# Kernel optimization log

Hardware: AMD Instinct MI355X
Metric: run time of the kernel (lower is better)

The kernel has to match this reference:

```python
import jax, jax.numpy as jnp
import numpy as np

S, B, C = 7, 2, 20
LAMBDA_COORD = 5.0
LAMBDA_NOOBJ = 0.5
EPS = 1e-6


def setup_inputs() -> dict:
    key = jax.random.key(0)
    k1, k2 = jax.random.split(key)
    N = 16384
    predictions = jax.random.normal(k1, (N, S, S, B * 5 + C), dtype=jnp.float32)
    targets = jax.random.normal(k2, (N, S, S, B * 5 + C), dtype=jnp.float32)
    return {"predictions": predictions, "targets": targets}


def _iou(b1, b2):
    # b1: [..., B, 4], b2: [..., 1, 4]; boxes are (x, y, w, h)
    b1x1 = b1[..., 0] - b1[..., 2] / 2
    b1y1 = b1[..., 1] - b1[..., 3] / 2
    b1x2 = b1[..., 0] + b1[..., 2] / 2
    b1y2 = b1[..., 1] + b1[..., 3] / 2
    b2x1 = b2[..., 0] - b2[..., 2] / 2
    b2y1 = b2[..., 1] - b2[..., 3] / 2
    b2x2 = b2[..., 0] + b2[..., 2] / 2
    b2y2 = b2[..., 1] + b2[..., 3] / 2
    inter = jnp.clip(jnp.minimum(b1x2, b2x2) - jnp.maximum(b1x1, b2x1), 0, None) * \
            jnp.clip(jnp.minimum(b1y2, b2y2) - jnp.maximum(b1y1, b2y1), 0, None)
    union = b1[..., 2] * b1[..., 3] + b2[..., 2] * b2[..., 3] - inter
    return inter / (union + EPS)


def reference(predictions, targets):
    N = predictions.shape[0]
    pred_boxes = predictions[..., : B * 5].reshape(N, S, S, B, 5)  # [N,S,S,B,5]
    tgt_box = targets[..., :5]                                     # [N,S,S,5]

    ious = _iou(pred_boxes[..., :4], tgt_box[..., None, :4])       # [N,S,S,B]
    # Replicate loop semantics: best starts at (iou=0, idx=0), strict '>' update
    best_idx = jnp.argmax(jnp.where(ious > 0, ious, 0.0), axis=-1)  # [N,S,S]
    best_box = jnp.take_along_axis(
        pred_boxes, best_idx[..., None, None], axis=3
    )[..., 0, :]                                                    # [N,S,S,5]

    obj = (tgt_box[..., 4] > 0).astype(predictions.dtype)          # [N,S,S]

    # Localization loss
    xy_err = jnp.sum((best_box[..., :2] - tgt_box[..., :2]) ** 2, axis=-1)
    wh_err = jnp.sum(
        (jnp.sqrt(jnp.clip(best_box[..., 2:4], EPS, None)) -
         jnp.sqrt(jnp.clip(tgt_box[..., 2:4], EPS, None))) ** 2, axis=-1)
    coord_loss = jnp.sum(obj * (xy_err + wh_err)) / N

    # Confidence losses
    conf_obj_loss = jnp.sum(obj * (best_box[..., 4] - tgt_box[..., 4]) ** 2) / N
    conf_sq = pred_boxes[..., 4] ** 2                              # [N,S,S,B]
    conf_sq_all = jnp.sum(conf_sq, axis=-1)
    conf_sq_best = jnp.take_along_axis(conf_sq, best_idx[..., None], axis=-1)[..., 0]
    conf_noobj_loss = jnp.sum(obj * (conf_sq_all - conf_sq_best) +
                              (1.0 - obj) * conf_sq_all) / N

    # Classification loss (only for object cells)
    cls_err = jnp.sum((predictions[..., B * 5:] - targets[..., B * 5:]) ** 2, axis=-1)
    class_loss = jnp.sum(obj * cls_err) / N

    total = (LAMBDA_COORD * coord_loss + conf_obj_loss +
             LAMBDA_NOOBJ * conf_noobj_loss + class_loss)
    return total
```

## Files before the change

### kernel.cpp

```cpp
#include <hip/hip_runtime.h>


constexpr float LC   = 5.0f;
constexpr float LN   = 0.5f;
constexpr float EPSF = 1e-6f;

__device__ __forceinline__ float iou_pair(
    float cx1, float cy1, float w1, float h1,
    float cx2, float cy2, float w2, float h2) {
  float b1x1 = cx1 - w1 * 0.5f, b1x2 = cx1 + w1 * 0.5f;
  float b1y1 = cy1 - h1 * 0.5f, b1y2 = cy1 + h1 * 0.5f;
  float b2x1 = cx2 - w2 * 0.5f, b2x2 = cx2 + w2 * 0.5f;
  float b2y1 = cy2 - h2 * 0.5f, b2y2 = cy2 + h2 * 0.5f;
  float iw = fmaxf(fminf(b1x2, b2x2) - fmaxf(b1x1, b2x1), 0.0f);
  float ih = fmaxf(fminf(b1y2, b2y2) - fmaxf(b1y1, b2y1), 0.0f);
  float inter = iw * ih;
  float uni = w1 * h1 + w2 * h2 - inter;
  return inter / (uni + EPSF);
}

__global__ __launch_bounds__(256) void yolo_win_kernel(
    const float* __restrict__ pred, const float* __restrict__ tgt,
    float* __restrict__ partial, float invN) {
  const int tid  = threadIdx.x;
  const int cell = blockIdx.x * 256 + tid;
  const int odd  = cell & 1;

  const size_t wbase = (size_t)cell * 30 - 2 * odd;
  const float4* p4 = (const float4*)(pred + wbase);
  const float4* t4 = (const float4*)(tgt + wbase);

  float4 P0 = p4[0], P1 = p4[1], P2 = p4[2], P3 = p4[3];
  float4 P4_ = p4[4], P5 = p4[5], P6 = p4[6], P7 = p4[7];
  float4 T0 = t4[0], T1 = t4[1], T2 = t4[2], T3 = t4[3];
  float4 T4_ = t4[4], T5 = t4[5], T6 = t4[6], T7 = t4[7];

  float wp[32] = {P0.x,P0.y,P0.z,P0.w, P1.x,P1.y,P1.z,P1.w,
                  P2.x,P2.y,P2.z,P2.w, P3.x,P3.y,P3.z,P3.w,
                  P4_.x,P4_.y,P4_.z,P4_.w, P5.x,P5.y,P5.z,P5.w,
                  P6.x,P6.y,P6.z,P6.w, P7.x,P7.y,P7.z,P7.w};
  float wt[32] = {T0.x,T0.y,T0.z,T0.w, T1.x,T1.y,T1.z,T1.w,
                  T2.x,T2.y,T2.z,T2.w, T3.x,T3.y,T3.z,T3.w,
                  T4_.x,T4_.y,T4_.z,T4_.w, T5.x,T5.y,T5.z,T5.w,
                  T6.x,T6.y,T6.z,T6.w, T7.x,T7.y,T7.z,T7.w};

  float d2[32];
#pragma unroll
  for (int k = 0; k < 32; ++k) {
    float d = wp[k] - wt[k];
    d2[k] = d * d;
  }

  float s0 = (d2[0]+d2[1]) + (d2[2]+d2[3]);
  float s1 = (d2[4]+d2[5]) + (d2[6]+d2[7]);
  float s2 = (d2[8]+d2[9]) + (d2[10]+d2[11]);
  float s3 = (d2[12]+d2[13]) + (d2[14]+d2[15]);
  float s4 = (d2[16]+d2[17]) + (d2[18]+d2[19]);
  float s5 = (d2[20]+d2[21]) + (d2[22]+d2[23]);
  float s6 = (d2[24]+d2[25]) + (d2[26]+d2[27]);
  float s7 = (d2[28]+d2[29]) + (d2[30]+d2[31]);
  float total32 = ((s0+s1)+(s2+s3)) + ((s4+s5)+(s6+s7));

  float common = ((d2[0]+d2[1]) + (d2[2]+d2[3])) +
                 ((d2[4]+d2[5]) + (d2[6]+d2[7])) + (d2[8]+d2[9]);
  float extra  = odd ? (d2[10] + d2[11]) : (d2[30] + d2[31]);
  float cls = total32 - common - extra;

  float p0 = odd ? wp[2]  : wp[0];
  float p1 = odd ? wp[3]  : wp[1];
  float p2 = odd ? wp[4]  : wp[2];
  float p3 = odd ? wp[5]  : wp[3];
  float p4v= odd ? wp[6]  : wp[4];
  float p5 = odd ? wp[7]  : wp[5];
  float p6 = odd ? wp[8]  : wp[6];
  float p7 = odd ? wp[9]  : wp[7];
  float p8 = odd ? wp[10] : wp[8];
  float p9 = odd ? wp[11] : wp[9];
  float t0 = odd ? wt[2]  : wt[0];
  float t1 = odd ? wt[3]  : wt[1];
  float t2 = odd ? wt[4]  : wt[2];
  float t3 = odd ? wt[5]  : wt[3];
  float t4v= odd ? wt[6]  : wt[4];

  float iou0 = iou_pair(p0, p1, p2, p3, t0, t1, t2, t3);
  float iou1 = iou_pair(p5, p6, p7, p8, t0, t1, t2, t3);
  float v0 = iou0 > 0.0f ? iou0 : 0.0f;
  float v1 = iou1 > 0.0f ? iou1 : 0.0f;
  bool pick1 = v1 > v0;

  float bx = pick1 ? p5 : p0;
  float by = pick1 ? p6 : p1;
  float bw = pick1 ? p7 : p2;
  float bh = pick1 ? p8 : p3;
  float bc = pick1 ? p9 : p4v;

  float obj = t4v > 0.0f ? 1.0f : 0.0f;

  float dx = bx - t0, dy = by - t1;
  float xy = dx * dx + dy * dy;
  float sw = sqrtf(fmaxf(bw, EPSF)) - sqrtf(fmaxf(t2, EPSF));
  float sh = sqrtf(fmaxf(bh, EPSF)) - sqrtf(fmaxf(t3, EPSF));
  float wh = sw * sw + sh * sh;
  float dc = bc - t4v;

  float sq0 = p4v * p4v, sq1 = p9 * p9;
  float sq_all  = sq0 + sq1;
  float sq_best = pick1 ? sq1 : sq0;
  float noobj = obj * (sq_all - sq_best) + (1.0f - obj) * sq_all;

  float contrib = (obj * (LC * (xy + wh) + dc * dc + cls) + LN * noobj) * invN;

  for (int off = 32; off > 0; off >>= 1)
    contrib += __shfl_down(contrib, off);
  __shared__ float wsum[4];
  int lane = tid & 63;
  int wid  = tid >> 6;
  if (lane == 0) wsum[wid] = contrib;
  __syncthreads();
  if (tid == 0)
    partial[blockIdx.x] = (wsum[0] + wsum[1]) + (wsum[2] + wsum[3]);
}

__global__ __launch_bounds__(256) void yolo_final_kernel(
    const float* __restrict__ partial, int n, float* __restrict__ out) {
  double s = 0.0;
  for (int i = threadIdx.x; i < n; i += 256) s += (double)partial[i];
  for (int off = 32; off > 0; off >>= 1) s += __shfl_down(s, off);
  __shared__ double wsum[4];
  int lane = threadIdx.x & 63;
  int wid  = threadIdx.x >> 6;
  if (lane == 0) wsum[wid] = s;
  __syncthreads();
  if (threadIdx.x == 0)
    out[0] = (float)((wsum[0] + wsum[1]) + (wsum[2] + wsum[3]));
}

extern "C" void kernel_launch(void* const* d_in, const int* in_sizes, int n_in,
                              void* d_out, int out_size, void* d_ws, size_t ws_size,
                              hipStream_t stream) {
  const float* pred = (const float*)d_in[0];
  const float* tgt  = (const float*)d_in[1];
  float* out = (float*)d_out;
  float* partial = (float*)d_ws;

  int ncells  = in_sizes[0] / 30;
  int nblocks = ncells / 256;
  int N       = ncells / 49;
  float invN  = 1.0f / (float)N;

  yolo_win_kernel<<<nblocks, 256, 0, stream>>>(pred, tgt, partial, invN);
  yolo_final_kernel<<<1, 256, 0, stream>>>(partial, nblocks, out);
}
```

Before: 39.91 us.

## Split each cell's 32-float window across two lanes with shuffle-combined class sum

Each cell is now handled by two adjacent threads. Each thread loads half of the 128-byte window (four float4 from each input), and the two partial class-error sums are combined with a lane shuffle. Only the even lane computes the IoU and box loss terms. This doubles the thread count and halves per-thread loads and registers, aiming for more memory-level parallelism, at the cost of idle lanes during the box math and twice as many blocks and partials.

```diff
diff --git a/kernel.cpp b/kernel.cpp
--- a/kernel.cpp
+++ b/kernel.cpp
@@ -19,96 +19,94 @@
   return inter / (uni + EPSF);
 }
 
-__global__ __launch_bounds__(256) void yolo_win_kernel(
+__global__ __launch_bounds__(256) void yolo_duo_kernel(
     const float* __restrict__ pred, const float* __restrict__ tgt,
     float* __restrict__ partial, float invN) {
   const int tid  = threadIdx.x;
-  const int cell = blockIdx.x * 256 + tid;
+  const int gid  = blockIdx.x * 256 + tid;
+  const int s    = gid & 1;
+  const int cell = gid >> 1;
   const int odd  = cell & 1;
 
   const size_t wbase = (size_t)cell * 30 - 2 * odd;
-  const float4* p4 = (const float4*)(pred + wbase);
-  const float4* t4 = (const float4*)(tgt + wbase);
+  const float4* p4 = (const float4*)(pred + wbase) + 4 * s;
+  const float4* t4 = (const float4*)(tgt + wbase) + 4 * s;
 
   float4 P0 = p4[0], P1 = p4[1], P2 = p4[2], P3 = p4[3];
-  float4 P4_ = p4[4], P5 = p4[5], P6 = p4[6], P7 = p4[7];
   float4 T0 = t4[0], T1 = t4[1], T2 = t4[2], T3 = t4[3];
-  float4 T4_ = t4[4], T5 = t4[5], T6 = t4[6], T7 = t4[7];
 
-  float wp[32] = {P0.x,P0.y,P0.z,P0.w, P1.x,P1.y,P1.z,P1.w,
-                  P2.x,P2.y,P2.z,P2.w, P3.x,P3.y,P3.z,P3.w,
-                  P4_.x,P4_.y,P4_.z,P4_.w, P5.x,P5.y,P5.z,P5.w,
-                  P6.x,P6.y,P6.z,P6.w, P7.x,P7.y,P7.z,P7.w};
-  float wt[32] = {T0.x,T0.y,T0.z,T0.w, T1.x,T1.y,T1.z,T1.w,
-                  T2.x,T2.y,T2.z,T2.w, T3.x,T3.y,T3.z,T3.w,
-                  T4_.x,T4_.y,T4_.z,T4_.w, T5.x,T5.y,T5.z,T5.w,
-                  T6.x,T6.y,T6.z,T6.w, T7.x,T7.y,T7.z,T7.w};
+  float wp[16] = {P0.x,P0.y,P0.z,P0.w, P1.x,P1.y,P1.z,P1.w,
+                  P2.x,P2.y,P2.z,P2.w, P3.x,P3.y,P3.z,P3.w};
+  float wt[16] = {T0.x,T0.y,T0.z,T0.w, T1.x,T1.y,T1.z,T1.w,
+                  T2.x,T2.y,T2.z,T2.w, T3.x,T3.y,T3.z,T3.w};
 
-  float d2[32];
+  float d2[16];
 #pragma unroll
-  for (int k = 0; k < 32; ++k) {
+  for (int k = 0; k < 16; ++k) {
     float d = wp[k] - wt[k];
     d2[k] = d * d;
   }
 
-  float s0 = (d2[0]+d2[1]) + (d2[2]+d2[3]);
-  float s1 = (d2[4]+d2[5]) + (d2[6]+d2[7]);
-  float s2 = (d2[8]+d2[9]) + (d2[10]+d2[11]);
-  float s3 = (d2[12]+d2[13]) + (d2[14]+d2[15]);
-  float s4 = (d2[16]+d2[17]) + (d2[18]+d2[19]);
-  float s5 = (d2[20]+d2[21]) + (d2[22]+d2[23]);
-  float s6 = (d2[24]+d2[25]) + (d2[26]+d2[27]);
-  float s7 = (d2[28]+d2[29]) + (d2[30]+d2[31]);
-  float total32 = ((s0+s1)+(s2+s3)) + ((s4+s5)+(s6+s7));
+  float cls_part;
+  {
+    float hi6 = ((d2[10] + d2[11]) + (d2[12] + d2[13])) + (d2[14] + d2[15]);
+    float cls0 = odd ? (hi6 - d2[10] - d2[11]) : hi6;
+    float s0 = (d2[0] + d2[1]) + (d2[2] + d2[3]);
+    float s1 = (d2[4] + d2[5]) + (d2[6] + d2[7]);
+    float s2 = (d2[8] + d2[9]) + (d2[10] + d2[11]);
+    float s3 = (d2[12] + d2[13]) + (d2[14] + d2[15]);
+    float all16 = (s0 + s1) + (s2 + s3);
+    float cls1 = odd ? all16 : (all16 - d2[14] - d2[15]);
+    cls_part = s ? cls1 : cls0;
+  }
+  float cls = cls_part + __shfl_down(cls_part, 1);
 
-  float common = ((d2[0]+d2[1]) + (d2[2]+d2[3])) +
-                 ((d2[4]+d2[5]) + (d2[6]+d2[7])) + (d2[8]+d2[9]);
-  float extra  = odd ? (d2[10] + d2[11]) : (d2[30] + d2[31]);
-  float cls = total32 - common - extra;
+  float contrib = 0.0f;
+  if (s == 0) {
+    float p0 = odd ? wp[2]  : wp[0];
+    float p1 = odd ? wp[3]  : wp[1];
+    float p2 = odd ? wp[4]  : wp[2];
+    float p3 = odd ? wp[5]  : wp[3];
+    float p4v= odd ? wp[6]  : wp[4];
+    float p5 = odd ? wp[7]  : wp[5];
+    float p6 = odd ? wp[8]  : wp[6];
+    float p7 = odd ? wp[9]  : wp[7];
+    float p8 = odd ? wp[10] : wp[8];
+    float p9 = odd ? wp[11] : wp[9];
+    float t0 = odd ? wt[2]  : wt[0];
+    float t1 = odd ? wt[3]  : wt[1];
+    float t2 = odd ? wt[4]  : wt[2];
+    float t3 = odd ? wt[5]  : wt[3];
+    float t4v= odd ? wt[6]  : wt[4];
 
-  float p0 = odd ? wp[2]  : wp[0];
-  float p1 = odd ? wp[3]  : wp[1];
-  float p2 = odd ? wp[4]  : wp[2];
-  float p3 = odd ? wp[5]  : wp[3];
-  float p4v= odd ? wp[6]  : wp[4];
-  float p5 = odd ? wp[7]  : wp[5];
-  float p6 = odd ? wp[8]  : wp[6];
-  float p7 = odd ? wp[9]  : wp[7];
-  float p8 = odd ? wp[10] : wp[8];
-  float p9 = odd ? wp[11] : wp[9];
-  float t0 = odd ? wt[2]  : wt[0];
-  float t1 = odd ? wt[3]  : wt[1];
-  float t2 = odd ? wt[4]  : wt[2];
-  float t3 = odd ? wt[5]  : wt[3];
-  float t4v= odd ? wt[6]  : wt[4];
+    float iou0 = iou_pair(p0, p1, p2, p3, t0, t1, t2, t3);
+    float iou1 = iou_pair(p5, p6, p7, p8, t0, t1, t2, t3);
+    float v0 = iou0 > 0.0f ? iou0 : 0.0f;
+    float v1 = iou1 > 0.0f ? iou1 : 0.0f;
+    bool pick1 = v1 > v0;
 
-  float iou0 = iou_pair(p0, p1, p2, p3, t0, t1, t2, t3);
-  float iou1 = iou_pair(p5, p6, p7, p8, t0, t1, t2, t3);
-  float v0 = iou0 > 0.0f ? iou0 : 0.0f;
-  float v1 = iou1 > 0.0f ? iou1 : 0.0f;
-  bool pick1 = v1 > v0;
+    float bx = pick1 ? p5 : p0;
+    float by = pick1 ? p6 : p1;
+    float bw = pick1 ? p7 : p2;
+    float bh = pick1 ? p8 : p3;
+    float bc = pick1 ? p9 : p4v;
 
-  float bx = pick1 ? p5 : p0;
-  float by = pick1 ? p6 : p1;
-  float bw = pick1 ? p7 : p2;
-  float bh = pick1 ? p8 : p3;
-  float bc = pick1 ? p9 : p4v;
+    float obj = t4v > 0.0f ? 1.0f : 0.0f;
 
-  float obj = t4v > 0.0f ? 1.0f : 0.0f;
+    float dx = bx - t0, dy = by - t1;
+    float xy = dx * dx + dy * dy;
+    float sw = sqrtf(fmaxf(bw, EPSF)) - sqrtf(fmaxf(t2, EPSF));
+    float sh = sqrtf(fmaxf(bh, EPSF)) - sqrtf(fmaxf(t3, EPSF));
+    float wh = sw * sw + sh * sh;
+    float dc = bc - t4v;
 
-  float dx = bx - t0, dy = by - t1;
-  float xy = dx * dx + dy * dy;
-  float sw = sqrtf(fmaxf(bw, EPSF)) - sqrtf(fmaxf(t2, EPSF));
-  float sh = sqrtf(fmaxf(bh, EPSF)) - sqrtf(fmaxf(t3, EPSF));
-  float wh = sw * sw + sh * sh;
-  float dc = bc - t4v;
+    float sq0 = p4v * p4v, sq1 = p9 * p9;
+    float sq_all  = sq0 + sq1;
+    float sq_best = pick1 ? sq1 : sq0;
+    float noobj = obj * (sq_all - sq_best) + (1.0f - obj) * sq_all;
 
-  float sq0 = p4v * p4v, sq1 = p9 * p9;
-  float sq_all  = sq0 + sq1;
-  float sq_best = pick1 ? sq1 : sq0;
-  float noobj = obj * (sq_all - sq_best) + (1.0f - obj) * sq_all;
-
-  float contrib = (obj * (LC * (xy + wh) + dc * dc + cls) + LN * noobj) * invN;
+    contrib = (obj * (LC * (xy + wh) + dc * dc + cls) + LN * noobj) * invN;
+  }
 
   for (int off = 32; off > 0; off >>= 1)
     contrib += __shfl_down(contrib, off);
@@ -144,10 +142,10 @@
   float* partial = (float*)d_ws;
 
   int ncells  = in_sizes[0] / 30;
-  int nblocks = ncells / 256;
+  int nblocks = ncells * 2 / 256;
   int N       = ncells / 49;
   float invN  = 1.0f / (float)N;
 
-  yolo_win_kernel<<<nblocks, 256, 0, stream>>>(pred, tgt, partial, invN);
+  yolo_duo_kernel<<<nblocks, 256, 0, stream>>>(pred, tgt, partial, invN);
   yolo_final_kernel<<<1, 256, 0, stream>>>(partial, nblocks, out);
 }
```

Result: no change. 39.66 us (-0.6%).
